# Performance work log

Measured on AMD Instinct MI355X. Metric: run time of the kernel, lower is better.

## Reference

```python
import jax, jax.numpy as jnp
import numpy as np

N_E = 8192
E_DIM = 64
BETA = 0.25
N_TOKENS = 32768


def setup_inputs() -> dict:
    key = jax.random.key(0)
    k1, k2 = jax.random.split(key)
    x = jax.random.normal(k1, (N_TOKENS, E_DIM), dtype=jnp.float32)
    # nn.Embedding weight initialized uniform(-1/n_e, 1/n_e)
    codebook = jax.random.uniform(k2, (N_E, E_DIM), dtype=jnp.float32,
                                  minval=-1.0 / N_E, maxval=1.0 / N_E)
    return {"x": x, "codebook": codebook, "start": 0, "end": N_E, "use_sk": 0}


def reference(x, codebook, start, end, use_sk):
    # use_sk=0 -> argmin branch (sinkhorn branch calls external helper, not exercised)
    latent = x.reshape(-1, E_DIM)                       # [N, D]
    cb = codebook[start:end]                            # [K, D]
    # squared euclidean distances: ||z||^2 + ||e||^2 - 2 z.e
    d = (jnp.sum(latent * latent, axis=1, keepdims=True)
         + jnp.sum(cb * cb, axis=1)[None, :]
         - 2.0 * jnp.einsum('nd,kd->nk', latent, cb))   # [N, K]
    indices = jnp.argmin(d, axis=-1) + start            # [N]
    x_q = codebook[indices].reshape(x.shape)            # gather
    sg = jax.lax.stop_gradient
    commitment_loss = jnp.mean((sg(x_q) - x) ** 2)
    codebook_loss = jnp.mean((x_q - sg(x)) ** 2)
    loss = codebook_loss + BETA * commitment_loss
    x_q_st = x + sg(x_q - x)                            # straight-through estimator
    indices = indices.reshape(x.shape[:-1])
    return x_q_st, loss, indices
```

## Files before the change

### kernel.cpp

```cpp
#include <hip/hip_runtime.h>
#include <math.h>


#define N_E    8192
#define EDIM   64
#define NTOK   32768
#define NELEM  (NTOK * EDIM)
#define CSZ    32
#define WINDOW 3e-4f
#define TTOK   256
#define TCODE  1024
#define SROW   72
#define TOKB   16
#define CCAP   64
#define KCAP   320

typedef __attribute__((ext_vector_type(8)))  short          short8;
typedef __attribute__((ext_vector_type(8)))  unsigned short ushort8v;
typedef __attribute__((ext_vector_type(16))) float          f32x16;

__device__ __forceinline__ unsigned short f2bf(float f) {
  unsigned int u = __float_as_uint(f);
  return (unsigned short)((u + 0x7FFFu + ((u >> 16) & 1u)) >> 16);
}
__device__ __forceinline__ unsigned short f2h(float f) {
  union { _Float16 h; unsigned short u; } cv; cv.h = (_Float16)f; return cv.u;
}
__device__ __forceinline__ float h2f(unsigned short b) {
  union { _Float16 h; unsigned short u; } cv; cv.u = b; return (float)cv.h;
}
__device__ __forceinline__ float max16(const f32x16 a) {
  float m = fmaxf(fmaxf(a[0], a[1]), a[2]);
  m = fmaxf(fmaxf(m, a[3]),  a[4]);
  m = fmaxf(fmaxf(m, a[5]),  a[6]);
  m = fmaxf(fmaxf(m, a[7]),  a[8]);
  m = fmaxf(fmaxf(m, a[9]),  a[10]);
  m = fmaxf(fmaxf(m, a[11]), a[12]);
  m = fmaxf(fmaxf(m, a[13]), a[14]);
  return fmaxf(m, a[15]);
}
__device__ __forceinline__ float sx_of(const float4* xl4) {
#pragma clang fp contract(off)
  float a0=0,a1=0,a2=0,a3=0,a4=0,a5=0,a6=0,a7=0;
#pragma unroll
  for (int i = 0; i < 8; ++i) {
    float4 pA = xl4[2*i], pB = xl4[2*i+1];
    a0 += pA.x * pA.x; a1 += pA.y * pA.y; a2 += pA.z * pA.z; a3 += pA.w * pA.w;
    a4 += pB.x * pB.x; a5 += pB.y * pB.y; a6 += pB.z * pB.z; a7 += pB.w * pB.w;
  }
  return ((a0+a1) + (a2+a3)) + ((a4+a5) + (a6+a7));
}

__global__ __launch_bounds__(256) void vq_sc(const float* __restrict__ cb,
                                             float* __restrict__ sc,
                                             unsigned short* __restrict__ cbf) {
#pragma clang fp contract(off)
  int r = blockIdx.x * 256 + threadIdx.x;
  const float4* c4 = (const float4*)(cb + (size_t)r * EDIM);
  float sval = sx_of(c4);
  sc[r] = sval;
  unsigned short* dst = cbf + (size_t)r * EDIM;
#pragma unroll
  for (int h = 0; h < 8; ++h) {
    float4 fA = c4[2*h], fB = c4[2*h+1];
    ushort8v o = {f2bf(fA.x), f2bf(fA.y), f2bf(fA.z), f2bf(fA.w),
                  f2bf(fB.x), f2bf(fB.y), f2bf(fB.z), f2bf(fB.w)};
    *(ushort8v*)&dst[h * 8] = o;
  }
}

__global__ __launch_bounds__(256, 3) void vq_pass1(
    const float* __restrict__ x, const unsigned short* __restrict__ cbf,
    unsigned int* __restrict__ cand, unsigned int* __restrict__ bmapb,
    const int* __restrict__ p_start, const int* __restrict__ p_end) {
  __shared__ unsigned short Cs[128 * SROW];
  int tid = threadIdx.x;
  int tb = blockIdx.x;
  int cbk = blockIdx.y;
  int s = *p_start, e = *p_end;
  const bool allfull = (cbk * TCODE >= s) && (cbk * TCODE + TCODE <= e);

  int lane = tid & 63, wv = tid >> 6;
  int half = lane >> 5, ln = lane & 31;
  int tokbase = wv * 64;

  const ushort8v* cg0 = (const ushort8v*)(cbf + (size_t)cbk * TCODE * EDIM);
#pragma unroll
  for (int p = 0; p < 4; ++p) {
    int idx = tid + p * 256;
    int row = idx >> 3, h = idx & 7;
    *(ushort8v*)&Cs[row * SROW + h * 8] = cg0[idx];
  }

  short8 bfr[2][4];
#pragma unroll
  for (int tg = 0; tg < 2; ++tg) {
    const float* xrow =
        x + (size_t)(tb * TTOK + tokbase + tg * 32 + ln) * EDIM + half * 8;
#pragma unroll
    for (int ks = 0; ks < 4; ++ks) {
      float4 fA = *(const float4*)(xrow + ks * 16);
      float4 fB = *(const float4*)(xrow + ks * 16 + 4);
      short8 v = {(short)f2bf(fA.x), (short)f2bf(fA.y), (short)f2bf(fA.z),
                  (short)f2bf(fA.w), (short)f2bf(fB.x), (short)f2bf(fB.y),
                  (short)f2bf(fB.z), (short)f2bf(fB.w)};
      bfr[tg][ks] = v;
    }
  }
  __syncthreads();

  unsigned s0=~0u,s1=~0u,s2=~0u,s3=~0u,s4=~0u,s5=~0u,s6=~0u,s7=~0u,s8=~0u;
  unsigned m0=0,m1=0,m2=0,m3=0,m4=0,m5=0,m6=0,m7=0,m8=0;
  unsigned bmap = 0u;
  float lm0 = INFINITY, lm1 = INFINITY;

  for (int nb = 0; nb < 8; ++nb) {
    ushort8v creg[4];
    if (nb < 7) {
      const ushort8v* cg =
          (const ushort8v*)(cbf + ((size_t)cbk * TCODE + (nb + 1) * 128) * EDIM);
#pragma unroll
      for (int p = 0; p < 4; ++p) creg[p] = cg[tid + p * 256];
    }
#pragma unroll
    for (int cp = 0; cp < 2; ++cp) {
      f32x16 acc[2][2];
#pragma unroll
      for (int tg = 0; tg < 2; ++tg)
#pragma unroll
        for (int c2 = 0; c2 < 2; ++c2) acc[tg][c2] = (f32x16)0.0f;
#pragma unroll
      for (int ks = 0; ks < 4; ++ks)
#pragma unroll
        for (int c2 = 0; c2 < 2; ++c2) {
          int ct = cp * 2 + c2;
          short8 a = *(const short8*)&Cs[(ct*32 + ln) * SROW + ks*16 + half*8];
          acc[0][c2] = __builtin_amdgcn_mfma_f32_32x32x16_bf16(a, bfr[0][ks],
                                                               acc[0][c2], 0, 0, 0);
          acc[1][c2] = __builtin_amdgcn_mfma_f32_32x32x16_bf16(a, bfr[1][ks],
                                                               acc[1][c2], 0, 0, 0);
        }
#pragma unroll
      for (int c2 = 0; c2 < 2; ++c2) {
        int cidL = nb * 4 + cp * 2 + c2;
        float v0, v1;
        if (allfull) {
          v0 = max16(acc[0][c2]);
          v1 = max16(acc[1][c2]);
        } else {
          int c0 = cbk * TCODE + cidL * 32;
          bool full = (c0 >= s) && (c0 + 32 <= e);
          if (full) {
            v0 = max16(acc[0][c2]);
            v1 = max16(acc[1][c2]);
          } else {
            v0 = -INFINITY; v1 = -INFINITY;
#pragma unroll
            for (int r = 0; r < 16; ++r) {
              int code = c0 + (r & 3) + 8 * (r >> 2) + 4 * half;
              if (code >= s && code < e) {
                v0 = fmaxf(v0, acc[0][c2][r]);
                v1 = fmaxf(v1, acc[1][c2][r]);
              }
            }
          }
        }
        v0 = fmaxf(v0, __shfl_xor(v0, 32, 64));
        v1 = fmaxf(v1, __shfl_xor(v1, 32, 64));
        unsigned short hh0 = f2h(-2.0f * v0);
        unsigned short hh1 = f2h(-2.0f * v1);
        float mv0 = h2f(hh0), mv1 = h2f(hh1);
        lm0 = fminf(lm0, mv0);
        lm1 = fminf(lm1, mv1);
        bool a0 = (mv0 <= lm0 + WINDOW);
        bool a1 = (mv1 <= lm1 + WINDOW);
        unsigned b0 = 0, b1 = 0;
        if (a0 | a1) {
          float t0 = v0 - WINDOW * 0.5f;
          float t1 = v1 - WINDOW * 0.5f;
#pragma unroll
          for (int r = 0; r < 16; ++r) {
            int pos = (r & 3) + 8 * (r >> 2) + 4 * half;
            if (acc[0][c2][r] >= t0) b0 |= (1u << pos);
            if (acc[1][c2][r] >= t1) b1 |= (1u << pos);
          }
          b0 |= __shfl_xor(b0, 32, 64);
          b1 |= __shfl_xor(b1, 32, 64);
        }
        bool aown = half ? a1 : a0;
        if (aown) {
          bmap |= 1u << cidL;
          unsigned short hh = half ? hh1 : hh0;
          unsigned bs = half ? b1 : b0;
          unsigned mono = (unsigned)hh ^ ((hh & 0x8000u) ? 0xFFFFu : 0x8000u);
          unsigned p = (mono << 16) | (unsigned)cidL;
          unsigned pm = bs;
          if (p < s8) {
#define INS2_(SK, SM) { bool lt_ = p < (SK); unsigned tk_ = (SK), tm_ = (SM); \
            if (lt_) { (SK) = p; (SM) = pm; p = tk_; pm = tm_; } }
            INS2_(s0,m0) INS2_(s1,m1) INS2_(s2,m2) INS2_(s3,m3) INS2_(s4,m4)
            INS2_(s5,m5) INS2_(s6,m6) INS2_(s7,m7) INS2_(s8,m8)
#undef INS2_
          }
        }
      }
    }
    __syncthreads();
    if (nb < 7) {
#pragma unroll
      for (int p = 0; p < 4; ++p) {
        int idx = tid + p * 256;
        int row = idx >> 3, h = idx & 7;
        *(ushort8v*)&Cs[row * SROW + h * 8] = creg[p];
      }
    }
    __syncthreads();
  }

  {
    float lminf = half ? lm1 : lm0;
    float thr = lminf + WINDOW;
    unsigned rec[8], msk[8];
#define EMIT_(J, S, M) { unsigned mono_ = (S) >> 16; \
    unsigned hh_ = (mono_ & 0x8000u) ? (mono_ ^ 0x8000u) : (mono_ ^ 0xFFFFu); \
    float v_ = h2f((unsigned short)hh_); \
    rec[J] = (v_ <= thr) ? ((hh_ << 16) | ((S) & 0xFFFFu)) : 0xFFFFFFFFu; \
    msk[J] = (M); }
    EMIT_(0, s0, m0) EMIT_(1, s1, m1) EMIT_(2, s2, m2) EMIT_(3, s3, m3)
    EMIT_(4, s4, m4) EMIT_(5, s5, m5) EMIT_(6, s6, m6) EMIT_(7, s7, m7)
#undef EMIT_
    {
      unsigned mono_ = s8 >> 16;
      unsigned hh_ = (mono_ & 0x8000u) ? (mono_ ^ 0x8000u) : (mono_ ^ 0xFFFFu);
      float v8 = h2f((unsigned short)hh_);
      if (v8 <= thr) rec[7] |= 0x8000u;
    }
    unsigned* eb = (unsigned*)Cs;
#pragma unroll
    for (int j = 0; j < 8; ++j) {
      eb[tid * 17 + j]     = rec[j];
      eb[tid * 17 + 8 + j] = msk[j];
    }
    bmapb[(size_t)cbk * NTOK + (tb * TTOK + tid)] = bmap;
  }
  __syncthreads();
#pragma unroll
  for (int p = 0; p < 4; ++p) {
    int idx = tid + p * 256;
    int tl = idx >> 2, part = idx & 3;
    const unsigned* src = (const unsigned*)Cs + tl * 17 + part * 4;
    uint4 v; v.x = src[0]; v.y = src[1]; v.z = src[2]; v.w = src[3];
    *(uint4*)(cand + (((size_t)(tb * TTOK + tl)) * 8 + cbk) * 16 + part * 4) = v;
  }
}

__global__ __launch_bounds__(256) void vq_rescue(
    const float* __restrict__ x, const float* __restrict__ cb,
    const float* __restrict__ sc, const unsigned int* __restrict__ cand,
    const unsigned int* __restrict__ bmapb,
    float* __restrict__ out_xq, float* __restrict__ out_idx,
    float* __restrict__ partial,
    const int* __restrict__ p_start, const int* __restrict__ p_end) {
#pragma clang fp contract(off)
  __shared__ float xsh[TOKB][64];
  __shared__ float sxs[TOKB];
  __shared__ unsigned short lst[TOKB][CCAP];
  __shared__ unsigned short clst[TOKB][KCAP];
  __shared__ int ccnt[TOKB], kcnt[TOKB];
  int tid  = threadIdx.x;
  int wv   = tid >> 6;
  int lane = tid & 63;
  int blk  = blockIdx.x;
  int s = *p_start, e = *p_end;

  if (tid < TOKB) { ccnt[tid] = 0; kcnt[tid] = 0; }
#pragma unroll
  for (int p = 0; p < (TOKB * CCAP) / 256; ++p)
    ((unsigned short*)lst)[tid + p * 256] = 0xFFFFu;
  __syncthreads();

  if (tid < 128) {
    int tl = tid >> 3, q = tid & 7;
    int gtok = blk * TOKB + tl;
    const uint4* rp = (const uint4*)(cand + ((size_t)gtok * 8 + q) * 16);
    uint4 A0 = rp[0], A1 = rp[1], M0 = rp[2], M1 = rp[3];
    unsigned rv[8] = {A0.x, A0.y, A0.z, A0.w, A1.x, A1.y, A1.z, A1.w};
    unsigned mk[8] = {M0.x, M0.y, M0.z, M0.w, M1.x, M1.y, M1.z, M1.w};
    float m = INFINITY;
#pragma unroll
    for (int j = 0; j < 8; ++j)
      m = fminf(m, h2f((unsigned short)(rv[j] >> 16)));
    m = fminf(m, __shfl_xor(m, 1, 64));
    m = fminf(m, __shfl_xor(m, 2, 64));
    m = fminf(m, __shfl_xor(m, 4, 64));
    float thr = m + WINDOW;
    bool marker = (rv[7] != 0xFFFFFFFFu) && ((rv[7] & 0x8000u) != 0u);
    unsigned slotbits = 0u;
#pragma unroll
    for (int j = 0; j < 8; ++j) {
      if (rv[j] != 0xFFFFFFFFu) {
        unsigned cid = rv[j] & 0x1Fu;
        slotbits |= 1u << cid;
        if (h2f((unsigned short)(rv[j] >> 16)) <= thr) {
          unsigned bits = mk[j];
          int n = __popc(bits);
          int base = atomicAdd(&ccnt[tl], n);
          if (base + n <= CCAP) {
            int kb = (q * 32 + (int)cid) * CSZ;
            while (bits) {
              int bpos = __ffs(bits) - 1; bits &= bits - 1;
              lst[tl][base++] = (unsigned short)(kb + bpos);
            }
          } else {
            int kb2 = atomicAdd(&kcnt[tl], 1);
            if (kb2 < KCAP) clst[tl][kb2] = (unsigned short)(q * 32 + (int)cid);
          }
        }
      }
    }
    if (marker) {
      unsigned bm = bmapb[(size_t)q * NTOK + gtok] & ~slotbits;
      int n = __popc(bm);
      int base = atomicAdd(&kcnt[tl], n);
      while (bm) {
        int j = __ffs(bm) - 1; bm &= bm - 1;
        if (base < KCAP) clst[tl][base] = (unsigned short)(q * 32 + j);
        ++base;
      }
    }
  } else if (tid < 192) {
    int t = tid - 128;
#pragma unroll
    for (int p = 0; p < 4; ++p) {
      int idx = t + p * 64;
      int tl = idx >> 4, seg = idx & 15;
      *(float4*)&xsh[tl][seg * 4] =
          ((const float4*)(x + (size_t)(blk * TOKB + tl) * EDIM))[seg];
    }
  } else if (tid < 192 + TOKB) {
    int tl = tid - 192;
    sxs[tl] = sx_of((const float4*)(x + (size_t)(blk * TOKB + tl) * EDIM));
  }
  __syncthreads();

#define EVAL_CODE_BODY(K_, XL4) do {                                           \
    const float4* c4_ = (const float4*)(cb + (size_t)(K_) * EDIM);             \
    float t0_=0.0f,t1_=0.0f,t2_=0.0f,t3_=0.0f;                                 \
    _Pragma("unroll")                                                          \
    for (int i_ = 0; i_ < 8; ++i_) {                 \
      float4 v_ = c4_[2*i_ + h5_];                                             \
      float4 p_ = (XL4)[2*i_ + h5_];                                           \
      t0_ += v_.x * p_.x; t1_ += v_.y * p_.y;                                  \
      t2_ += v_.z * p_.z; t3_ += v_.w * p_.w;                                  \
    }                                                                          \
    s2_ = (t0_ + t1_) + (t2_ + t3_);              \
  } while (0)

#define FINISH_CODE(K_, ACT, SX, BP) do {                                      \
    float tt_ = s2_ + __shfl_xor(s2_, 1, 64);                                  \
    if ((ACT) && (K_) >= s && (K_) < e) {                                      \
      float d_ = ((SX) + sc[K_]) - 2.0f * tt_;                                 \
      unsigned db_ = __float_as_uint(d_);                                      \
      unsigned en_ = db_ ^ ((unsigned)((int)db_ >> 31) | 0x80000000u);         \
      unsigned long long pk_ = ((unsigned long long)en_ << 32) | (unsigned)(K_);\
      if (pk_ < (BP)) (BP) = pk_;                                              \
    }                                                                          \
  } while (0)

  float sg[4];
#pragma unroll
  for (int ti = 0; ti < 4; ++ti) {
    int tl = wv * 4 + ti;
    int gtok = blk * TOKB + tl;
    const float4* xl4 = (const float4*)xsh[tl];
    float sx = sxs[tl];
    unsigned long long bp = ~0ull;
    int ci_ = lane >> 1, h5_ = lane & 1;
    int nc = ccnt[tl]; if (nc > CCAP) nc = CCAP;
    for (int b0 = 0; b0 < nc; b0 += 32) {
      int nb = nc - b0; if (nb > 32) nb = 32;
      int kraw = (ci_ < nb) ? (int)lst[tl][b0 + ci_] : 0xFFFF;
      bool act = (kraw != 0xFFFF);
      int k_ = act ? kraw : 0;
      float s2_ = 0.0f;
      if (act) EVAL_CODE_BODY(k_, xl4);
      FINISH_CODE(k_, act, sx, bp);
    }
    int nk = kcnt[tl]; if (nk > KCAP) nk = KCAP;
    for (int i = 0; i < nk; ++i) {
      int k_ = (int)clst[tl][i] * CSZ + ci_;
      float s2_;
      EVAL_CODE_BODY(k_, xl4);
      FINISH_CODE(k_, true, sx, bp);
    }
#pragma unroll
    for (int off = 32; off >= 1; off >>= 1) {
      unsigned long long o = __shfl_xor(bp, off, 64);
      if (o < bp) bp = o;
    }
    int bidx = (int)(unsigned)(bp & 0xFFFFFFFFull) & (N_E - 1);

    float xx = xsh[tl][lane];
    float qv = cb[(size_t)bidx * EDIM + lane];
    float diff = qv - xx;
    out_xq[(size_t)gtok * EDIM + lane] = xx + diff;
    if (lane == 0) out_idx[gtok] = (float)bidx;
    float l = diff * diff;
#pragma unroll
    for (int off = 32; off >= 1; off >>= 1) l += __shfl_down(l, off, 64);
    sg[ti] = l;
  }
#undef EVAL_CODE_BODY
#undef FINISH_CODE
  if (lane == 0)
    partial[blk * 4 + wv] = (sg[0] + sg[1]) + (sg[2] + sg[3]);
}

__global__ __launch_bounds__(256) void vq_loss(const float* __restrict__ partial,
                                               float* __restrict__ out_loss) {
  int tid = threadIdx.x;
  float s = 0.0f;
  for (int i = tid; i < NTOK / 4; i += 256) s += partial[i];
#pragma unroll
  for (int off = 32; off >= 1; off >>= 1) s += __shfl_down(s, off, 64);
  __shared__ float sdata[4];
  if ((tid & 63) == 0) sdata[tid >> 6] = s;
  __syncthreads();
  if (tid == 0) {
    float total = (sdata[0] + sdata[1]) + (sdata[2] + sdata[3]);
    float m = total * (1.0f / (float)NELEM);
    out_loss[0] = m + 0.25f * m;
  }
}

extern "C" void kernel_launch(void* const* d_in, const int* in_sizes, int n_in,
                              void* d_out, int out_size, void* d_ws, size_t ws_size,
                              hipStream_t stream) {
  const float* x  = (const float*)d_in[0];
  const float* cb = (const float*)d_in[1];
  const int* p_start = (const int*)d_in[2];
  const int* p_end   = (const int*)d_in[3];

  float* ws = (float*)d_ws;
  float* sc      = ws;
  float* partial = ws + N_E;
  unsigned short* cbf  = (unsigned short*)(ws + 2 * N_E);
  unsigned int*   cand = (unsigned int*)(cbf + (size_t)N_E * EDIM);
  unsigned int*   bmapb = cand + (size_t)NTOK * 8 * 16;

  float* out      = (float*)d_out;
  float* out_xq   = out;
  float* out_loss = out + NELEM;
  float* out_idx  = out + NELEM + 1;

  vq_sc<<<N_E / 256, 256, 0, stream>>>(cb, sc, cbf);
  dim3 g1(NTOK / TTOK, N_E / TCODE);
  vq_pass1<<<g1, 256, 0, stream>>>(x, cbf, cand, bmapb, p_start, p_end);
  vq_rescue<<<NTOK / TOKB, 256, 0, stream>>>(x, cb, sc, cand, bmapb, out_xq, out_idx,
                                             partial, p_start, p_end);
  vq_loss<<<1, 256, 0, stream>>>(partial, out_loss);
}
```

Before: 186.1 us.

## Halve tokens per pass1 block to cut registers and raise occupancy

Reduces the pass1 token tile from 256 to 128 so each wave handles one 32-token MFMA group instead of two, dropping the duplicated accumulators and per-half bookkeeping, and raises launch bounds to 4 blocks per CU. The intent is to lower register pressure, increase occupancy and double the grid so latency is better hidden. In exchange, each codebook tile loaded into LDS is reused by half as many tokens, doubling codebook traffic per token, and half the lanes idle during the final emit.

```diff
diff --git a/kernel.cpp b/kernel.cpp
--- a/kernel.cpp
+++ b/kernel.cpp
@@ -8,7 +8,7 @@
 #define NELEM  (NTOK * EDIM)
 #define CSZ    32
 #define WINDOW 3e-4f
-#define TTOK   256
+#define TTOK   128
 #define TCODE  1024
 #define SROW   72
 #define TOKB   16
@@ -69,7 +69,7 @@
   }
 }
 
-__global__ __launch_bounds__(256, 3) void vq_pass1(
+__global__ __launch_bounds__(256, 4) void vq_pass1(
     const float* __restrict__ x, const unsigned short* __restrict__ cbf,
     unsigned int* __restrict__ cand, unsigned int* __restrict__ bmapb,
     const int* __restrict__ p_start, const int* __restrict__ p_end) {
@@ -82,7 +82,7 @@
 
   int lane = tid & 63, wv = tid >> 6;
   int half = lane >> 5, ln = lane & 31;
-  int tokbase = wv * 64;
+  int tokbase = wv * 32;
 
   const ushort8v* cg0 = (const ushort8v*)(cbf + (size_t)cbk * TCODE * EDIM);
 #pragma unroll
@@ -92,11 +92,10 @@
     *(ushort8v*)&Cs[row * SROW + h * 8] = cg0[idx];
   }
 
-  short8 bfr[2][4];
-#pragma unroll
-  for (int tg = 0; tg < 2; ++tg) {
+  short8 bfr[4];
+  {
     const float* xrow =
-        x + (size_t)(tb * TTOK + tokbase + tg * 32 + ln) * EDIM + half * 8;
+        x + (size_t)(tb * TTOK + tokbase + ln) * EDIM + half * 8;
 #pragma unroll
     for (int ks = 0; ks < 4; ++ks) {
       float4 fA = *(const float4*)(xrow + ks * 16);
@@ -104,7 +103,7 @@
       short8 v = {(short)f2bf(fA.x), (short)f2bf(fA.y), (short)f2bf(fA.z),
                   (short)f2bf(fA.w), (short)f2bf(fB.x), (short)f2bf(fB.y),
                   (short)f2bf(fB.z), (short)f2bf(fB.w)};
-      bfr[tg][ks] = v;
+      bfr[ks] = v;
     }
   }
   __syncthreads();
@@ -112,7 +111,7 @@
   unsigned s0=~0u,s1=~0u,s2=~0u,s3=~0u,s4=~0u,s5=~0u,s6=~0u,s7=~0u,s8=~0u;
   unsigned m0=0,m1=0,m2=0,m3=0,m4=0,m5=0,m6=0,m7=0,m8=0;
   unsigned bmap = 0u;
-  float lm0 = INFINITY, lm1 = INFINITY;
+  float lm = INFINITY;
 
   for (int nb = 0; nb < 8; ++nb) {
     ushort8v creg[4];
@@ -124,77 +123,55 @@
     }
 #pragma unroll
     for (int cp = 0; cp < 2; ++cp) {
-      f32x16 acc[2][2];
-#pragma unroll
-      for (int tg = 0; tg < 2; ++tg)
-#pragma unroll
-        for (int c2 = 0; c2 < 2; ++c2) acc[tg][c2] = (f32x16)0.0f;
+      f32x16 acc[2];
+#pragma unroll
+      for (int c2 = 0; c2 < 2; ++c2) acc[c2] = (f32x16)0.0f;
 #pragma unroll
       for (int ks = 0; ks < 4; ++ks)
 #pragma unroll
         for (int c2 = 0; c2 < 2; ++c2) {
           int ct = cp * 2 + c2;
           short8 a = *(const short8*)&Cs[(ct*32 + ln) * SROW + ks*16 + half*8];
-          acc[0][c2] = __builtin_amdgcn_mfma_f32_32x32x16_bf16(a, bfr[0][ks],
-                                                               acc[0][c2], 0, 0, 0);
-          acc[1][c2] = __builtin_amdgcn_mfma_f32_32x32x16_bf16(a, bfr[1][ks],
-                                                               acc[1][c2], 0, 0, 0);
+          acc[c2] = __builtin_amdgcn_mfma_f32_32x32x16_bf16(a, bfr[ks],
+                                                            acc[c2], 0, 0, 0);
         }
 #pragma unroll
       for (int c2 = 0; c2 < 2; ++c2) {
         int cidL = nb * 4 + cp * 2 + c2;
-        float v0, v1;
+        float v;
         if (allfull) {
-          v0 = max16(acc[0][c2]);
-          v1 = max16(acc[1][c2]);
+          v = max16(acc[c2]);
         } else {
           int c0 = cbk * TCODE + cidL * 32;
           bool full = (c0 >= s) && (c0 + 32 <= e);
           if (full) {
-            v0 = max16(acc[0][c2]);
-            v1 = max16(acc[1][c2]);
+            v = max16(acc[c2]);
           } else {
-            v0 = -INFINITY; v1 = -INFINITY;
+            v = -INFINITY;
 #pragma unroll
             for (int r = 0; r < 16; ++r) {
               int code = c0 + (r & 3) + 8 * (r >> 2) + 4 * half;
-              if (code >= s && code < e) {
-                v0 = fmaxf(v0, acc[0][c2][r]);
-                v1 = fmaxf(v1, acc[1][c2][r]);
-              }
+              if (code >= s && code < e) v = fmaxf(v, acc[c2][r]);
             }
           }
         }
-        v0 = fmaxf(v0, __shfl_xor(v0, 32, 64));
-        v1 = fmaxf(v1, __shfl_xor(v1, 32, 64));
-        unsigned short hh0 = f2h(-2.0f * v0);
-        unsigned short hh1 = f2h(-2.0f * v1);
-        float mv0 = h2f(hh0), mv1 = h2f(hh1);
-        lm0 = fminf(lm0, mv0);
-        lm1 = fminf(lm1, mv1);
-        bool a0 = (mv0 <= lm0 + WINDOW);
-        bool a1 = (mv1 <= lm1 + WINDOW);
-        unsigned b0 = 0, b1 = 0;
-        if (a0 | a1) {
-          float t0 = v0 - WINDOW * 0.5f;
-          float t1 = v1 - WINDOW * 0.5f;
+        v = fmaxf(v, __shfl_xor(v, 32, 64));
+        unsigned short hh = f2h(-2.0f * v);
+        float mv = h2f(hh);
+        lm = fminf(lm, mv);
+        if (mv <= lm + WINDOW) {
+          bmap |= 1u << cidL;
+          float t = v - WINDOW * 0.5f;
+          unsigned b = 0;
 #pragma unroll
           for (int r = 0; r < 16; ++r) {
             int pos = (r & 3) + 8 * (r >> 2) + 4 * half;
-            if (acc[0][c2][r] >= t0) b0 |= (1u << pos);
-            if (acc[1][c2][r] >= t1) b1 |= (1u << pos);
+            if (acc[c2][r] >= t) b |= (1u << pos);
           }
-          b0 |= __shfl_xor(b0, 32, 64);
-          b1 |= __shfl_xor(b1, 32, 64);
-        }
-        bool aown = half ? a1 : a0;
-        if (aown) {
-          bmap |= 1u << cidL;
-          unsigned short hh = half ? hh1 : hh0;
-          unsigned bs = half ? b1 : b0;
+          b |= __shfl_xor(b, 32, 64);
           unsigned mono = (unsigned)hh ^ ((hh & 0x8000u) ? 0xFFFFu : 0x8000u);
           unsigned p = (mono << 16) | (unsigned)cidL;
-          unsigned pm = bs;
+          unsigned pm = b;
           if (p < s8) {
 #define INS2_(SK, SM) { bool lt_ = p < (SK); unsigned tk_ = (SK), tm_ = (SM); \
             if (lt_) { (SK) = p; (SM) = pm; p = tk_; pm = tm_; } }
@@ -217,9 +194,8 @@
     __syncthreads();
   }
 
-  {
-    float lminf = half ? lm1 : lm0;
-    float thr = lminf + WINDOW;
+  if (!half) {
+    float thr = lm + WINDOW;
     unsigned rec[8], msk[8];
 #define EMIT_(J, S, M) { unsigned mono_ = (S) >> 16; \
     unsigned hh_ = (mono_ & 0x8000u) ? (mono_ ^ 0x8000u) : (mono_ ^ 0xFFFFu); \
@@ -235,17 +211,18 @@
       float v8 = h2f((unsigned short)hh_);
       if (v8 <= thr) rec[7] |= 0x8000u;
     }
+    int tl = tokbase + ln;
     unsigned* eb = (unsigned*)Cs;
 #pragma unroll
     for (int j = 0; j < 8; ++j) {
-      eb[tid * 17 + j]     = rec[j];
-      eb[tid * 17 + 8 + j] = msk[j];
-    }
-    bmapb[(size_t)cbk * NTOK + (tb * TTOK + tid)] = bmap;
+      eb[tl * 17 + j]     = rec[j];
+      eb[tl * 17 + 8 + j] = msk[j];
+    }
+    bmapb[(size_t)cbk * NTOK + (tb * TTOK + tl)] = bmap;
   }
   __syncthreads();
 #pragma unroll
-  for (int p = 0; p < 4; ++p) {
+  for (int p = 0; p < 2; ++p) {
     int idx = tid + p * 256;
     int tl = idx >> 2, part = idx & 3;
     const unsigned* src = (const unsigned*)Cs + tl * 17 + part * 4;
```

Result: faster. 181.2 us (-2.7%).
